# Optimization experiments

Measured on AMD Instinct MI355X. Metric: run time of the kernel, lower is better.

The kernel has to match this reference:

```python
import jax, jax.numpy as jnp
from jax import lax
import numpy as np

ORDER = 4        # Butterworth order -> ORDER//2 second-order sections
CUTOFF = 150.0   # Hz
FS = 48000.0     # Hz
B, C, T = 32, 8, 96000


def _butter_lowpass_sos(order: int, cutoff: float, fs: float) -> np.ndarray:
    """Butterworth lowpass design (bilinear transform), SOS output (n_sections, 6).
    Same math as scipy.signal.butter(..., output='sos') up to per-section gain
    distribution (each section normalized to unity DC gain)."""
    assert order % 2 == 0
    warped = 2.0 * fs * np.tan(np.pi * cutoff / fs)  # prewarped analog cutoff
    k = np.arange(order // 2)
    theta = np.pi / 2.0 + np.pi * (2 * k + 1) / (2.0 * order)  # upper-half-plane poles
    p = warped * np.exp(1j * theta)
    fs2 = 2.0 * fs
    z = (fs2 + p) / (fs2 - p)  # bilinear-transformed digital poles
    a1 = -2.0 * z.real
    a2 = np.abs(z) ** 2
    g = (1.0 + a1 + a2) / 4.0  # unity DC gain per section; zeros at z=-1 -> num [1,2,1]
    sos = np.stack([g, 2.0 * g, g, np.ones_like(g), a1, a2], axis=1)
    return sos.astype(np.float32)


def setup_inputs() -> dict:
    key = jax.random.key(0)
    x = jax.random.normal(key, (B, C, T), dtype=jnp.float32)
    sos = jnp.asarray(_butter_lowpass_sos(ORDER, CUTOFF, FS))  # (2, 6)
    return {"x": x, "sos": sos}


def _apply_section(x_nt, b0, b1, b2, a1, a2):
    """Direct Form II biquad over time for all signals in parallel. x_nt: (N, T)."""
    n = x_nt.shape[0]

    def step(carry, x_n):
        w1, w2 = carry
        w0 = x_n - a1 * w1 - a2 * w2
        y_n = b0 * w0 + b1 * w1 + b2 * w2
        return (w0, w1), y_n

    init = (jnp.zeros((n,), x_nt.dtype), jnp.zeros((n,), x_nt.dtype))
    _, y_tn = lax.scan(step, init, x_nt.T)  # scan over T, vectorized over N
    return y_tn.T


def reference(x, sos):
    orig_shape = x.shape
    xf = x.reshape(-1, orig_shape[-1])  # (B*C, T)
    y = xf
    n_sections = sos.shape[0]
    for i in range(n_sections):  # small fixed count (2)
        a0 = sos[i, 3]
        y = _apply_section(
            y,
            sos[i, 0] / a0, sos[i, 1] / a0, sos[i, 2] / a0,
            sos[i, 4] / a0, sos[i, 5] / a0,
        )
    return y.reshape(orig_shape)
```

## Files before the change

### kernel.cpp

```cpp
#include <hip/hip_runtime.h>

#define NSIG   256
#define T_LEN  96000
#define NCHUNK 250
#define CLEN   384

struct Coefs {
  float b01, b11, b21, na11, na21;
  float b02, b12, b22, na12, na22;
};

__device__ __forceinline__ Coefs load_coefs(const float* __restrict__ sos) {
  Coefs c;
  float i0 = 1.0f / sos[3];
  c.b01 = sos[0] * i0; c.b11 = sos[1] * i0; c.b21 = sos[2] * i0;
  c.na11 = -sos[4] * i0; c.na21 = -sos[5] * i0;
  float i1 = 1.0f / sos[9];
  c.b02 = sos[6] * i1; c.b12 = sos[7] * i1; c.b22 = sos[8] * i1;
  c.na12 = -sos[10] * i1; c.na22 = -sos[11] * i1;
  return c;
}

__device__ __forceinline__ float step2(float xin, float& w11, float& w21,
                                       float& w12, float& w22, const Coefs& c) {
  float w0 = fmaf(c.na11, w11, fmaf(c.na21, w21, xin));
  float y1 = fmaf(c.b21, w21, fmaf(c.b11, w11, c.b01 * w0));
  w21 = w11; w11 = w0;
  float w0b = fmaf(c.na12, w12, fmaf(c.na22, w22, y1));
  float y2 = fmaf(c.b22, w22, fmaf(c.b12, w12, c.b02 * w0b));
  w22 = w12; w12 = w0b;
  return y2;
}

__global__ __launch_bounds__(256) void k_phase1(const float* __restrict__ x,
                                                const float* __restrict__ sos,
                                                float4* __restrict__ vzs) {
  int sig = blockIdx.x;
  int chk = threadIdx.x;
  if (chk >= NCHUNK) return;
  Coefs cf = load_coefs(sos);
  const float4* xp = reinterpret_cast<const float4*>(
      x + (size_t)sig * T_LEN + (size_t)chk * CLEN);
  float w11 = 0.f, w21 = 0.f, w12 = 0.f, w22 = 0.f;
#pragma unroll 8
  for (int j = 0; j < CLEN / 4; ++j) {
    float4 xv = xp[j];
    (void)step2(xv.x, w11, w21, w12, w22, cf);
    (void)step2(xv.y, w11, w21, w12, w22, cf);
    (void)step2(xv.z, w11, w21, w12, w22, cf);
    (void)step2(xv.w, w11, w21, w12, w22, cf);
  }
  float4 st; st.x = w11; st.y = w21; st.z = w12; st.w = w22;
  vzs[(size_t)chk * NSIG + sig] = st;
}

#define PF 10
__global__ __launch_bounds__(256) void k_scan(const float* __restrict__ sos,
                                              const float4* __restrict__ vzs,
                                              float4* __restrict__ vinit) {
  __shared__ float Ash[16];
  Coefs cf = load_coefs(sos);
  int t = threadIdx.x;
  if (t < 4) {
    float w11 = (t == 0) ? 1.f : 0.f;
    float w21 = (t == 1) ? 1.f : 0.f;
    float w12 = (t == 2) ? 1.f : 0.f;
    float w22 = (t == 3) ? 1.f : 0.f;
    for (int j = 0; j < CLEN; ++j)
      (void)step2(0.f, w11, w21, w12, w22, cf);
    Ash[0 * 4 + t] = w11; Ash[1 * 4 + t] = w21;
    Ash[2 * 4 + t] = w12; Ash[3 * 4 + t] = w22;
  }
  __syncthreads();
  float A[16];
#pragma unroll
  for (int i = 0; i < 16; ++i) A[i] = Ash[i];

  float4 zb[PF], zb2[PF];
#pragma unroll
  for (int i = 0; i < PF; ++i) zb[i] = vzs[(size_t)i * NSIG + t];
  float4 v; v.x = 0.f; v.y = 0.f; v.z = 0.f; v.w = 0.f;
  for (int g = 0; g < NCHUNK / PF; ++g) {
#pragma unroll
    for (int i = 0; i < PF; ++i) {
      int c2 = (g + 1) * PF + i;
      c2 = c2 < NCHUNK ? c2 : NCHUNK - 1;
      zb2[i] = vzs[(size_t)c2 * NSIG + t];
    }
#pragma unroll
    for (int i = 0; i < PF; ++i) {
      int c = g * PF + i;
      vinit[(size_t)c * NSIG + t] = v;
      float4 z = zb[i];
      float4 nv;
      nv.x = fmaf(A[ 3], v.w, fmaf(A[ 2], v.z, fmaf(A[ 1], v.y, fmaf(A[ 0], v.x, z.x))));
      nv.y = fmaf(A[ 7], v.w, fmaf(A[ 6], v.z, fmaf(A[ 5], v.y, fmaf(A[ 4], v.x, z.y))));
      nv.z = fmaf(A[11], v.w, fmaf(A[10], v.z, fmaf(A[ 9], v.y, fmaf(A[ 8], v.x, z.z))));
      nv.w = fmaf(A[15], v.w, fmaf(A[14], v.z, fmaf(A[13], v.y, fmaf(A[12], v.x, z.w))));
      v = nv;
    }
#pragma unroll
    for (int i = 0; i < PF; ++i) zb[i] = zb2[i];
  }
}

__global__ __launch_bounds__(256) void k_phase3(const float* __restrict__ x,
                                                const float* __restrict__ sos,
                                                const float4* __restrict__ vinit,
                                                float* __restrict__ y) {
  int sig = blockIdx.x;
  int chk = threadIdx.x;
  if (chk >= NCHUNK) return;
  Coefs cf = load_coefs(sos);
  size_t base = (size_t)sig * T_LEN + (size_t)chk * CLEN;
  const float4* xp = reinterpret_cast<const float4*>(x + base);
  float4* yp = reinterpret_cast<float4*>(y + base);
  float4 v = vinit[(size_t)chk * NSIG + sig];
  float w11 = v.x, w21 = v.y, w12 = v.z, w22 = v.w;
#pragma unroll 8
  for (int j = 0; j < CLEN / 4; ++j) {
    float4 xv = xp[j];
    float4 yv;
    yv.x = step2(xv.x, w11, w21, w12, w22, cf);
    yv.y = step2(xv.y, w11, w21, w12, w22, cf);
    yv.z = step2(xv.z, w11, w21, w12, w22, cf);
    yv.w = step2(xv.w, w11, w21, w12, w22, cf);
    yp[j] = yv;
  }
}

extern "C" void kernel_launch(void* const* d_in, const int* in_sizes, int n_in,
                              void* d_out, int out_size, void* d_ws, size_t ws_size,
                              hipStream_t stream) {
  const float* x   = (const float*)d_in[0];
  const float* sos = (const float*)d_in[1];
  float* yout = (float*)d_out;
  float4* vzs   = (float4*)d_ws;
  float4* vinit = vzs + (size_t)NCHUNK * NSIG;

  k_phase1<<<NSIG, 256, 0, stream>>>(x, sos, vzs);
  k_scan<<<1, 256, 0, stream>>>(sos, vzs, vinit);
  k_phase3<<<NSIG, 256, 0, stream>>>(x, sos, vinit, yout);
}
```

Baseline: 241.1 us.

## Stage input and output tiles through padded LDS for coalesced global access

```diff
diff --git a/kernel.cpp b/kernel.cpp
--- a/kernel.cpp
+++ b/kernel.cpp
@@ -4,6 +4,10 @@
 #define T_LEN  96000
 #define NCHUNK 250
 #define CLEN   384
+#define W      64
+#define NW     (CLEN / W)
+#define ROWF   (W + 1)
+#define TILE_F4 (NCHUNK * (W / 4))
 
 struct Coefs {
   float b01, b11, b21, na11, na21;
@@ -35,23 +39,31 @@
 __global__ __launch_bounds__(256) void k_phase1(const float* __restrict__ x,
                                                 const float* __restrict__ sos,
                                                 float4* __restrict__ vzs) {
-  int sig = blockIdx.x;
-  int chk = threadIdx.x;
-  if (chk >= NCHUNK) return;
+  __shared__ float xs[NCHUNK * ROWF];
+  int sig = blockIdx.x, tid = threadIdx.x;
   Coefs cf = load_coefs(sos);
-  const float4* xp = reinterpret_cast<const float4*>(
-      x + (size_t)sig * T_LEN + (size_t)chk * CLEN);
+  const float4* xg = reinterpret_cast<const float4*>(x) + (size_t)sig * (T_LEN / 4);
   float w11 = 0.f, w21 = 0.f, w12 = 0.f, w22 = 0.f;
+  for (int wi = 0; wi < NW; ++wi) {
+    __syncthreads();
+    for (int u = tid; u < TILE_F4; u += 256) {
+      int c = u >> 4, k4 = u & 15;
+      float4 v = xg[c * (CLEN / 4) + wi * (W / 4) + k4];
+      float* dst = &xs[c * ROWF + k4 * 4];
+      dst[0] = v.x; dst[1] = v.y; dst[2] = v.z; dst[3] = v.w;
+    }
+    __syncthreads();
+    if (tid < NCHUNK) {
+      const float* xr = &xs[tid * ROWF];
 #pragma unroll 8
-  for (int j = 0; j < CLEN / 4; ++j) {
-    float4 xv = xp[j];
-    (void)step2(xv.x, w11, w21, w12, w22, cf);
-    (void)step2(xv.y, w11, w21, w12, w22, cf);
-    (void)step2(xv.z, w11, w21, w12, w22, cf);
-    (void)step2(xv.w, w11, w21, w12, w22, cf);
+      for (int j = 0; j < W; ++j)
+        (void)step2(xr[j], w11, w21, w12, w22, cf);
+    }
   }
-  float4 st; st.x = w11; st.y = w21; st.z = w12; st.w = w22;
-  vzs[(size_t)chk * NSIG + sig] = st;
+  if (tid < NCHUNK) {
+    float4 st; st.x = w11; st.y = w21; st.z = w12; st.w = w22;
+    vzs[(size_t)tid * NSIG + sig] = st;
+  }
 }
 
 #define PF 10
@@ -108,24 +120,38 @@
                                                 const float* __restrict__ sos,
                                                 const float4* __restrict__ vinit,
                                                 float* __restrict__ y) {
-  int sig = blockIdx.x;
-  int chk = threadIdx.x;
-  if (chk >= NCHUNK) return;
+  __shared__ float ts[NCHUNK * ROWF];
+  int sig = blockIdx.x, tid = threadIdx.x;
   Coefs cf = load_coefs(sos);
-  size_t base = (size_t)sig * T_LEN + (size_t)chk * CLEN;
-  const float4* xp = reinterpret_cast<const float4*>(x + base);
-  float4* yp = reinterpret_cast<float4*>(y + base);
-  float4 v = vinit[(size_t)chk * NSIG + sig];
-  float w11 = v.x, w21 = v.y, w12 = v.z, w22 = v.w;
+  const float4* xg = reinterpret_cast<const float4*>(x) + (size_t)sig * (T_LEN / 4);
+  float4* yg = reinterpret_cast<float4*>(y) + (size_t)sig * (T_LEN / 4);
+  float w11 = 0.f, w21 = 0.f, w12 = 0.f, w22 = 0.f;
+  if (tid < NCHUNK) {
+    float4 v = vinit[(size_t)tid * NSIG + sig];
+    w11 = v.x; w21 = v.y; w12 = v.z; w22 = v.w;
+  }
+  for (int wi = 0; wi < NW; ++wi) {
+    __syncthreads();
+    for (int u = tid; u < TILE_F4; u += 256) {
+      int c = u >> 4, k4 = u & 15;
+      float4 v = xg[c * (CLEN / 4) + wi * (W / 4) + k4];
+      float* dst = &ts[c * ROWF + k4 * 4];
+      dst[0] = v.x; dst[1] = v.y; dst[2] = v.z; dst[3] = v.w;
+    }
+    __syncthreads();
+    if (tid < NCHUNK) {
+      float* xr = &ts[tid * ROWF];
 #pragma unroll 8
-  for (int j = 0; j < CLEN / 4; ++j) {
-    float4 xv = xp[j];
-    float4 yv;
-    yv.x = step2(xv.x, w11, w21, w12, w22, cf);
-    yv.y = step2(xv.y, w11, w21, w12, w22, cf);
-    yv.z = step2(xv.z, w11, w21, w12, w22, cf);
-    yv.w = step2(xv.w, w11, w21, w12, w22, cf);
-    yp[j] = yv;
+      for (int j = 0; j < W; ++j)
+        xr[j] = step2(xr[j], w11, w21, w12, w22, cf);
+    }
+    __syncthreads();
+    for (int u = tid; u < TILE_F4; u += 256) {
+      int c = u >> 4, k4 = u & 15;
+      const float* s = &ts[c * ROWF + k4 * 4];
+      float4 v; v.x = s[0]; v.y = s[1]; v.z = s[2]; v.w = s[3];
+      yg[c * (CLEN / 4) + wi * (W / 4) + k4] = v;
+    }
   }
 }
 
```

After: 253.7 us. 1.05x slower.
